# Performance work log

Hardware: AMD Instinct MI355X
Metric: run time of the kernel (lower is better)

The kernel has to match this reference:

```python
import jax, jax.numpy as jnp
import numpy as np

BN_EPS = 1e-6
SOFTMAX_EPS = 1e-8
D = 64      # fingerprint_dim
BD = 12     # bond_dim
N_ATOM = 10000
N_EDGE = 40000


def _bn(x, gamma, beta, mean, var):
    # BatchNorm1d in inference mode (running stats)
    return (x - mean) / jnp.sqrt(var + BN_EPS) * gamma + beta


def setup_inputs() -> dict:
    key = jax.random.key(0)
    ks = jax.random.split(key, 16)
    inp = {
        "atom": jax.random.normal(ks[0], (N_ATOM, D), dtype=jnp.float32),
        "bond_index": jax.random.randint(ks[1], (N_EDGE, 2), 0, N_ATOM, dtype=jnp.int64),
        "bond": jax.random.normal(ks[2], (N_EDGE, BD), dtype=jnp.float32),
        # encoder: Linear(bond_dim, D*D) + BatchNorm1d(D*D)
        "enc_W": jax.random.normal(ks[3], (D * D, BD), dtype=jnp.float32) * (1.0 / np.sqrt(BD)),
        "enc_b": jnp.zeros((D * D,), dtype=jnp.float32),
        "enc_gamma": jnp.ones((D * D,), dtype=jnp.float32),
        "enc_beta": jnp.zeros((D * D,), dtype=jnp.float32),
        "enc_mean": jnp.zeros((D * D,), dtype=jnp.float32),
        "enc_var": jnp.ones((D * D,), dtype=jnp.float32),
        # align: Linear(2*D, 1)
        "align_W": jax.random.normal(ks[4], (1, 2 * D), dtype=jnp.float32) * (1.0 / np.sqrt(2 * D)),
        "align_b": jnp.zeros((1,), dtype=jnp.float32),
        # attend: Linear(D, D) + BatchNorm1d(D), no activation
        "att_W": jax.random.normal(ks[5], (D, D), dtype=jnp.float32) * (1.0 / np.sqrt(D)),
        "att_b": jnp.zeros((D,), dtype=jnp.float32),
        "att_gamma": jnp.ones((D,), dtype=jnp.float32),
        "att_beta": jnp.zeros((D,), dtype=jnp.float32),
        "att_mean": jnp.zeros((D,), dtype=jnp.float32),
        "att_var": jnp.ones((D,), dtype=jnp.float32),
        # GRUCell(D, D)
        "gru_W_ih": jax.random.normal(ks[6], (3 * D, D), dtype=jnp.float32) * (1.0 / np.sqrt(D)),
        "gru_W_hh": jax.random.normal(ks[7], (3 * D, D), dtype=jnp.float32) * (1.0 / np.sqrt(D)),
        "gru_b_ih": jnp.zeros((3 * D,), dtype=jnp.float32),
        "gru_b_hh": jnp.zeros((3 * D,), dtype=jnp.float32),
    }
    return inp


def reference(atom, bond_index, bond,
              enc_W, enc_b, enc_gamma, enc_beta, enc_mean, enc_var,
              align_W, align_b,
              att_W, att_b, att_gamma, att_beta, att_mean, att_var,
              gru_W_ih, gru_W_hh, gru_b_ih, gru_b_hh):
    num_atom, d = atom.shape
    tgt = bond_index[:, 0]  # target atom of each edge
    nbr = bond_index[:, 1]  # neighbor atom of each edge

    # encoder: relu(BN(linear(bond))) -> per-edge [d, d] bond matrix
    enc = jax.nn.relu(_bn(bond @ enc_W.T + enc_b, enc_gamma, enc_beta, enc_mean, enc_var))
    enc = enc.reshape(-1, d, d)  # [E, d, d]

    # gather neighbor atoms, per-edge matvec through bond matrix
    neighbor = jnp.einsum('ed,edf->ef', atom[nbr], enc)  # [E, d]

    # attention logits (dropout is identity in eval)
    feat = jnp.concatenate([atom[tgt], neighbor], axis=-1)  # [E, 2d]
    score = jax.nn.leaky_relu(feat @ align_W.T + align_b, negative_slope=0.01)  # [E, 1]

    # segment softmax over target atoms
    mx = jax.ops.segment_max(score, tgt, num_segments=num_atom)  # [N, 1]
    ex = jnp.exp(score - mx[tgt])
    denom = jax.ops.segment_sum(ex, tgt, num_segments=num_atom)[tgt] + SOFTMAX_EPS
    attn = ex / denom  # [E, 1]

    # attend: BN(linear(neighbor)) (no activation), weighted scatter-add
    attd = _bn(neighbor @ att_W.T + att_b, att_gamma, att_beta, att_mean, att_var)
    context = jax.ops.segment_sum(attn * attd, tgt, num_segments=num_atom)  # [N, d]
    context = jax.nn.elu(context)

    # GRUCell(context, atom)
    gi = context @ gru_W_ih.T + gru_b_ih  # [N, 3d]
    gh = atom @ gru_W_hh.T + gru_b_hh     # [N, 3d]
    i_r, i_z, i_n = jnp.split(gi, 3, axis=-1)
    h_r, h_z, h_n = jnp.split(gh, 3, axis=-1)
    r = jax.nn.sigmoid(i_r + h_r)
    z = jax.nn.sigmoid(i_z + h_z)
    n = jnp.tanh(i_n + r * h_n)
    return (1.0 - z) * n + z * atom
```

## Files before the change

### kernel.cpp

```cpp
#include <hip/hip_runtime.h>
#include <math.h>

#define NA 10000
#define NE 40000

typedef float f4 __attribute__((ext_vector_type(4)));
typedef float f16v __attribute__((ext_vector_type(16)));
typedef int   i4 __attribute__((ext_vector_type(4)));
typedef __bf16 bf16x8 __attribute__((ext_vector_type(8)));

union U8 { unsigned short us[8]; bf16x8 v; };

static __device__ __forceinline__ unsigned short bf_rne(float x){
  unsigned u = __float_as_uint(x);
  unsigned r = (u + 0x7fffu + ((u>>16)&1u)) >> 16;
  return (unsigned short)r;
}
static __device__ __forceinline__ float bf_to_f(unsigned short h){
  return __uint_as_float(((unsigned)h)<<16);
}

__global__ __launch_bounds__(256) void k_pre(
  const float* __restrict__ encW, const float* __restrict__ encB,
  const float* __restrict__ eg, const float* __restrict__ ebt,
  const float* __restrict__ e_mn, const float* __restrict__ e_vr,
  const float* __restrict__ attW, const float* __restrict__ attB,
  const float* __restrict__ agm, const float* __restrict__ abt,
  const float* __restrict__ amn, const float* __restrict__ avr,
  const float* __restrict__ wih, const float* __restrict__ whh,
  const int* __restrict__ bidx, const float* __restrict__ atom,
  const float* __restrict__ alW,
  unsigned short* __restrict__ Bh, unsigned short* __restrict__ Bl,
  unsigned short* __restrict__ aBh, unsigned short* __restrict__ aBl,
  float* __restrict__ attBf, float* __restrict__ wT,
  float* __restrict__ p, int* __restrict__ cnt)
{
  int tid = threadIdx.x;
  int gid = blockIdx.x*256 + tid;
  int gstride = gridDim.x*256;
  for (int i=gid; i<65536; i+=gstride){
    int j = i&7, ll = (i>>3)&63, t = i>>9;
    int d = t>>1, ft = t&1;
    int k = ((ll>>5)<<3)+j;
    int n = d*64 + ft*32 + (ll&31);
    float s = eg[n]*rsqrtf(e_vr[n]+1e-6f);
    unsigned short vh=0, vl=0;
    if (k<12){
      float wv = encW[n*12+k]*s;
      unsigned short hi = bf_rne(wv);
      vh = hi; vl = bf_rne(wv - bf_to_f(hi));
    } else if (k==12){
      float b = (encB[n]-e_mn[n])*s + ebt[n];
      unsigned short hi = bf_rne(b);
      vh = hi; vl = bf_rne(b - bf_to_f(hi));
    }
    Bh[i] = vh; Bl[i] = vl;
  }
  for (int i=gid; i<4096; i+=gstride){
    int j=i&7, l=(i>>3)&63, t=i>>9;
    int kk=t>>1, nt=t&1;
    int k = kk*16 + ((l>>5)<<3) + j;
    int n = nt*32 + (l&31);
    float s = agm[n]*rsqrtf(avr[n]+1e-6f);
    float wv = attW[n*64+k]*s;
    unsigned short hi = bf_rne(wv);
    aBh[i]=hi; aBl[i]=bf_rne(wv - bf_to_f(hi));
  }
  for (int f=gid; f<64; f+=gstride){
    float s = agm[f]*rsqrtf(avr[f]+1e-6f);
    attBf[f] = (attB[f]-amn[f])*s + abt[f];
  }
  for (int i=gid; i<24576; i+=gstride){
    int j=i&3, f=(i>>2)&63, idx2=i>>8;
    int g=idx2>>4, kg=idx2&15, k=kg*4+j;
    wT[i] = (g<3)? wih[(g*64+f)*64+k] : whh[((g-3)*64+f)*64+k];
  }
  {
    int wid = gid>>6;
    int l = tid&63;
    float wl = alW[l];
    for (int a=wid; a<NA; a+=(gstride>>6)){
      float v = wl*atom[(size_t)a*64+l];
      v += __shfl_xor(v,1);  v += __shfl_xor(v,2);
      v += __shfl_xor(v,4);  v += __shfl_xor(v,8);
      v += __shfl_xor(v,16); v += __shfl_xor(v,32);
      if (l==0) p[a]=v;
    }
  }
  for (int e=gid; e<NE; e+=gstride) atomicAdd(&cnt[bidx[e*2]],1);
}

__global__ __launch_bounds__(256) void k_scan(const int* __restrict__ cnt,
                                              int* __restrict__ rowstart,
                                              int* __restrict__ wofs)
{
  __shared__ int sPart[256];
  int t = threadIdx.x;
  int base = t*40;
  i4 buf[10];
  int sum = 0;
  if (base < NA){
    const i4* cp = (const i4*)(cnt + base);
    #pragma unroll
    for (int i=0;i<10;i++) buf[i] = cp[i];
    #pragma unroll
    for (int i=0;i<10;i++) sum += buf[i].x+buf[i].y+buf[i].z+buf[i].w;
  }
  sPart[t]=sum;
  __syncthreads();
  for (int off=1; off<256; off<<=1){
    int v = (t>=off)? sPart[t-off] : 0;
    __syncthreads();
    sPart[t]+=v;
    __syncthreads();
  }
  int run = sPart[t]-sum;
  if (base < NA){
    #pragma unroll
    for (int i=0;i<10;i++){
      i4 b=buf[i], o;
      o.x=run; run+=b.x; o.y=run; run+=b.y;
      o.z=run; run+=b.z; o.w=run; run+=b.w;
      ((i4*)(rowstart+base))[i]=o;
      ((i4*)(wofs+base))[i]=o;
    }
  }
  if (t==0) rowstart[NA]=NE;
}

__global__ __launch_bounds__(256) void k_scatter(const int* __restrict__ bidx,
                                                 int* __restrict__ wofs,
                                                 int* __restrict__ elist)
{
  int e = blockIdx.x*256 + threadIdx.x;
  if (e < NE){
    int tg = bidx[e*2];
    int pos = atomicAdd(&wofs[tg],1);
    elist[pos]=e;
  }
}

__global__ __launch_bounds__(256) void k_edge(
  const float* __restrict__ atom, const int* __restrict__ bidx, const float* __restrict__ bond,
  const unsigned short* __restrict__ Bh, const unsigned short* __restrict__ Bl,
  const int* __restrict__ elist, float* __restrict__ nbC)
{
  __shared__ float sA[4352];
  __shared__ float sP[8192];
  __shared__ int   sEl[64];
  __shared__ int   sNbr[64];

  int tid = threadIdx.x;
  int l = tid & 63;
  int w = tid >> 6;
  int g = l >> 5;
  int em = l & 31;
  int E0 = blockIdx.x * 64;

  if (tid < 64){
    int e = elist[E0+tid];
    sEl[tid] = e;
    sNbr[tid] = bidx[e*2+1];
  }
  __syncthreads();
  for (int i=tid; i<4096; i+=256){
    int le=i>>6, d=i&63;
    sA[d*68+le] = atom[(size_t)sNbr[le]*64 + d];
  }

  U8 A1[2], A2[2];
  #pragma unroll
  for (int mt=0; mt<2; mt++){
    const f4* bp = (const f4*)(bond + (size_t)sEl[mt*32+em]*12);
    f4 b0=bp[0], b1v=bp[1], b2v=bp[2];
    float bv[12] = {b0.x,b0.y,b0.z,b0.w,b1v.x,b1v.y,b1v.z,b1v.w,b2v.x,b2v.y,b2v.z,b2v.w};
    unsigned short hi[12], lo2[12];
    #pragma unroll
    for (int j=0;j<12;j++){ hi[j]=bf_rne(bv[j]); lo2[j]=bf_rne(bv[j]-bf_to_f(hi[j])); }
    #pragma unroll
    for (int j=0;j<8;j++){
      int k = g*8+j;
      A1[mt].us[j] = (k<12)? hi[k] : (k==12? (unsigned short)0x3F80 : (unsigned short)0);
      A2[mt].us[j] = (k<12)? lo2[k] : (unsigned short)0;
    }
  }
  __syncthreads();

  f4 nacc[2][2][4];
  #pragma unroll
  for (int mt=0; mt<2; mt++)
    #pragma unroll
    for (int ft=0; ft<2; ft++)
      #pragma unroll
      for (int q=0;q<4;q++) nacc[mt][ft][q] = (f4){0.f,0.f,0.f,0.f};
  f16v cz;
  #pragma unroll
  for (int r=0;r<16;r++) cz[r] = 0.f;

  int dbase = w*16;
  U8 cbh0, cbl0, cbh1, cbl1;
  cbh0.v = *(const bf16x8*)(Bh + ((size_t)((dbase*2+0)*64 + l))*8);
  cbl0.v = *(const bf16x8*)(Bl + ((size_t)((dbase*2+0)*64 + l))*8);
  cbh1.v = *(const bf16x8*)(Bh + ((size_t)((dbase*2+1)*64 + l))*8);
  cbl1.v = *(const bf16x8*)(Bl + ((size_t)((dbase*2+1)*64 + l))*8);

  #pragma unroll 2
  for (int dd=0; dd<16; dd++){
    int d = dbase + dd;
    int dn = (dd<15)? d+1 : d;
    U8 nbh0, nbl0, nbh1, nbl1;
    nbh0.v = *(const bf16x8*)(Bh + ((size_t)((dn*2+0)*64 + l))*8);
    nbl0.v = *(const bf16x8*)(Bl + ((size_t)((dn*2+0)*64 + l))*8);
    nbh1.v = *(const bf16x8*)(Bh + ((size_t)((dn*2+1)*64 + l))*8);
    nbl1.v = *(const bf16x8*)(Bl + ((size_t)((dn*2+1)*64 + l))*8);

    #pragma unroll
    for (int mt=0; mt<2; mt++){
      f4 ldA[4];
      #pragma unroll
      for (int q=0;q<4;q++) ldA[q] = *(const f4*)&sA[d*68 + mt*32 + 8*q + 4*g];
      {
        f16v c;
        c = __builtin_amdgcn_mfma_f32_32x32x16_bf16(A1[mt].v, cbh0.v, cz, 0,0,0);
        c = __builtin_amdgcn_mfma_f32_32x32x16_bf16(A2[mt].v, cbh0.v, c, 0,0,0);
        c = __builtin_amdgcn_mfma_f32_32x32x16_bf16(A1[mt].v, cbl0.v, c, 0,0,0);
        #pragma unroll
        for (int r=0;r<16;r++){
          float ev = fmaxf(c[r], 0.f);
          nacc[mt][0][r>>2][r&3] = fmaf(ldA[r>>2][r&3], ev, nacc[mt][0][r>>2][r&3]);
        }
      }
      {
        f16v c;
        c = __builtin_amdgcn_mfma_f32_32x32x16_bf16(A1[mt].v, cbh1.v, cz, 0,0,0);
        c = __builtin_amdgcn_mfma_f32_32x32x16_bf16(A2[mt].v, cbh1.v, c, 0,0,0);
        c = __builtin_amdgcn_mfma_f32_32x32x16_bf16(A1[mt].v, cbl1.v, c, 0,0,0);
        #pragma unroll
        for (int r=0;r<16;r++){
          float ev = fmaxf(c[r], 0.f);
          nacc[mt][1][r>>2][r&3] = fmaf(ldA[r>>2][r&3], ev, nacc[mt][1][r>>2][r&3]);
        }
      }
    }
    cbh0 = nbh0; cbl0 = nbl0; cbh1 = nbh1; cbl1 = nbl1;
  }

  #pragma unroll
  for (int ft=0; ft<2; ft++){
    __syncthreads();
    #pragma unroll
    for (int mt=0; mt<2; mt++)
      #pragma unroll
      for (int r=0;r<16;r++)
        sP[w*2048 + mt*1024 + r*64 + l] = nacc[mt][ft][r>>2][r&3];
    __syncthreads();
    for (int idx=tid; idx<2048; idx+=256){
      float v = sP[idx] + sP[2048+idx] + sP[4096+idx] + sP[6144+idx];
      int mt = idx>>10, rl = idx&1023;
      int r = rl>>6, ll = rl&63;
      int m = mt*32 + (r&3) + ((r>>2)<<3) + ((ll>>5)<<2);
      int f = (ft<<5) + (ll&31);
      nbC[(size_t)(E0+m)*64 + f] = v;
    }
  }
}

__global__ __launch_bounds__(256) void k_zq(
  const float* __restrict__ nbC,
  const unsigned short* __restrict__ aBh, const unsigned short* __restrict__ aBl,
  const float* __restrict__ alW,
  float* __restrict__ zC, float* __restrict__ qv)
{
  __shared__ float sNb[64*68];
  int tid = threadIdx.x;
  int l = tid & 63;
  int w = tid >> 6;
  int g = l >> 5;
  int em = l & 31;
  int E0 = blockIdx.x * 64;

  for (int i=tid; i<4096; i+=256){
    int le=i>>6, f=i&63;
    sNb[le*68+f] = nbC[(size_t)(E0+le)*64 + f];
  }
  __syncthreads();

  {
    float alwn = alW[64+l];
    #pragma unroll 4
    for (int i=0;i<16;i++){
      int le = w*16 + i;
      float qq = sNb[le*68 + l] * alwn;
      qq += __shfl_xor(qq,1);  qq += __shfl_xor(qq,2);
      qq += __shfl_xor(qq,4);  qq += __shfl_xor(qq,8);
      qq += __shfl_xor(qq,16); qq += __shfl_xor(qq,32);
      if (l==0) qv[E0+le] = qq;
    }
  }

  {
    f16v c;
    #pragma unroll
    for (int r=0;r<16;r++) c[r] = 0.f;
    int mt2 = w>>1, nt = w&1;
    #pragma unroll
    for (int kk=0; kk<4; kk++){
      const float* src = &sNb[(mt2*32+em)*68 + kk*16 + g*8];
      f4 x0 = *(const f4*)src;
      f4 x1 = *(const f4*)(src+4);
      U8 Ah, Al;
      #pragma unroll
      for (int j=0;j<4;j++){
        unsigned short h0 = bf_rne(x0[j]);
        Ah.us[j] = h0; Al.us[j] = bf_rne(x0[j]-bf_to_f(h0));
        unsigned short h1 = bf_rne(x1[j]);
        Ah.us[4+j] = h1; Al.us[4+j] = bf_rne(x1[j]-bf_to_f(h1));
      }
      U8 bh, bl;
      bh.v = *(const bf16x8*)(aBh + ((size_t)((kk*2+nt)*64 + l))*8);
      bl.v = *(const bf16x8*)(aBl + ((size_t)((kk*2+nt)*64 + l))*8);
      c = __builtin_amdgcn_mfma_f32_32x32x16_bf16(Ah.v, bh.v, c, 0,0,0);
      c = __builtin_amdgcn_mfma_f32_32x32x16_bf16(Al.v, bh.v, c, 0,0,0);
      c = __builtin_amdgcn_mfma_f32_32x32x16_bf16(Ah.v, bl.v, c, 0,0,0);
    }
    #pragma unroll
    for (int r=0;r<16;r++){
      int row = (r&3) + ((r>>2)<<3) + ((l>>5)<<2);
      zC[(size_t)(E0 + mt2*32 + row)*64 + nt*32 + (l&31)] = c[r];
    }
  }
}

__global__ __launch_bounds__(256, 4) void k_gru(
  const float* __restrict__ atom, const float* __restrict__ zC,
  const int* __restrict__ rowstart, const float* __restrict__ p,
  const float* __restrict__ qv, const float* __restrict__ alB,
  const float* __restrict__ attBf, const float* __restrict__ wT,
  const float* __restrict__ bih, const float* __restrict__ bhh,
  float* __restrict__ out)
{
  __shared__ float sc[4][2][64];
  __shared__ float shh[4][2][64];
  int tid = threadIdx.x;
  int l = tid & 63;
  int w = tid >> 6;
  int base = blockIdx.x*8 + w*2;
  float bias = attBf[l];
  float ab = alB[0];

  #pragma unroll
  for (int aa=0; aa<2; aa++){
    int a = base + aa;
    float cf=0.f, hf=0.f;
    if (a < NA){
      hf = atom[(size_t)a*64 + l];
      int d0 = rowstart[a];
      int deg = rowstart[a+1] - d0;
      if (deg > 0){
        float pa = p[a] + ab;
        float mx = -1e30f;
        #pragma unroll 1
        for (int i=0;i<deg;i++){
          float s = pa + qv[d0+i];
          s = (s>0.f)? s : 0.01f*s;
          mx = fmaxf(mx, s);
        }
        float dn = 0.f, y = 0.f;
        #pragma unroll 1
        for (int i=0;i<deg;i++){
          float s = pa + qv[d0+i];
          s = (s>0.f)? s : 0.01f*s;
          float ex = __expf(s - mx);
          dn += ex;
          y = fmaf(ex, zC[(size_t)(d0+i)*64 + l], y);
        }
        cf = (y + dn*bias)/(dn + 1e-8f);
        cf = (cf>0.f)? cf : expm1f(cf);
      }
    }
    sc[w][aa][l] = cf; shh[w][aa][l] = hf;
  }
  __syncthreads();

  float acc[6][2];
  #pragma unroll
  for (int gg=0;gg<6;gg++){ acc[gg][0]=0.f; acc[gg][1]=0.f; }

  #pragma unroll 2
  for (int kg=0; kg<16; kg++){
    f4 wv[6];
    #pragma unroll
    for (int gg=0;gg<6;gg++) wv[gg] = *(const f4*)&wT[(size_t)((gg*16+kg)*64 + l)*4];
    #pragma unroll
    for (int aa=0;aa<2;aa++){
      f4 cv = *(const f4*)&sc[w][aa][kg*4];
      f4 hv = *(const f4*)&shh[w][aa][kg*4];
      #pragma unroll
      for (int j=0;j<4;j++){
        acc[0][aa] = fmaf(cv[j], wv[0][j], acc[0][aa]);
        acc[1][aa] = fmaf(cv[j], wv[1][j], acc[1][aa]);
        acc[2][aa] = fmaf(cv[j], wv[2][j], acc[2][aa]);
        acc[3][aa] = fmaf(hv[j], wv[3][j], acc[3][aa]);
        acc[4][aa] = fmaf(hv[j], wv[4][j], acc[4][aa]);
        acc[5][aa] = fmaf(hv[j], wv[5][j], acc[5][aa]);
      }
    }
  }

  float b0 = bih[l], b1 = bih[64+l], b2 = bih[128+l];
  float h0 = bhh[l], h1 = bhh[64+l], h2 = bhh[128+l];
  #pragma unroll
  for (int aa=0;aa<2;aa++){
    int a = base + aa;
    if (a < NA){
      float hf = shh[w][aa][l];
      float r = 1.f/(1.f + expf(-(acc[0][aa] + b0 + acc[3][aa] + h0)));
      float z = 1.f/(1.f + expf(-(acc[1][aa] + b1 + acc[4][aa] + h1)));
      float n = tanhf(acc[2][aa] + b2 + r*(acc[5][aa] + h2));
      out[(size_t)a*64 + l] = (1.f - z)*n + z*hf;
    }
  }
}

extern "C" void kernel_launch(void* const* d_in, const int* in_sizes, int n_in,
                              void* d_out, int out_size, void* d_ws, size_t ws_size,
                              hipStream_t stream) {
  const float* atom = (const float*)d_in[0];
  const int*   bidx = (const int*)  d_in[1];
  const float* bond = (const float*)d_in[2];
  const float* encW = (const float*)d_in[3];
  const float* encB = (const float*)d_in[4];
  const float* eg   = (const float*)d_in[5];
  const float* ebt  = (const float*)d_in[6];
  const float* e_mn = (const float*)d_in[7];
  const float* e_vr = (const float*)d_in[8];
  const float* alW  = (const float*)d_in[9];
  const float* alB  = (const float*)d_in[10];
  const float* atW  = (const float*)d_in[11];
  const float* atB  = (const float*)d_in[12];
  const float* agm  = (const float*)d_in[13];
  const float* abt  = (const float*)d_in[14];
  const float* amn  = (const float*)d_in[15];
  const float* avr  = (const float*)d_in[16];
  const float* wih  = (const float*)d_in[17];
  const float* whh  = (const float*)d_in[18];
  const float* bih  = (const float*)d_in[19];
  const float* bhh  = (const float*)d_in[20];

  float* ws = (float*)d_ws;
  unsigned short* Bh  = (unsigned short*)(ws + 0);
  unsigned short* Bl  = (unsigned short*)(ws + 32768);
  unsigned short* aBh = (unsigned short*)(ws + 65536);
  unsigned short* aBl = (unsigned short*)(ws + 67584);
  float* attBf   = ws + 69632;
  float* wT      = ws + 69696;
  float* p       = ws + 94272;
  int*   cnt     = (int*)(ws + 104288);
  int*   rowstart= (int*)(ws + 114304);
  int*   wofs    = (int*)(ws + 124320);
  int*   elist   = (int*)(ws + 134336);
  float* qv      = ws + 174336;
  float* nbC     = ws + 214336;
  float* outp    = (float*)d_out;

  hipMemsetAsync(cnt, 0, NA*sizeof(int), stream);
  k_pre<<<512, 256, 0, stream>>>(encW,encB,eg,ebt,e_mn,e_vr,
                                 atW,atB,agm,abt,amn,avr,
                                 wih,whh,bidx,atom,alW,
                                 Bh,Bl,aBh,aBl,attBf,wT,p,cnt);
  k_scan<<<1, 256, 0, stream>>>(cnt, rowstart, wofs);
  k_scatter<<<(NE+255)/256, 256, 0, stream>>>(bidx, wofs, elist);
  k_edge<<<625, 256, 0, stream>>>(atom, bidx, bond, Bh, Bl, elist, nbC);
  k_zq<<<625, 256, 0, stream>>>(nbC, aBh, aBl, alW, nbC , qv);
  k_gru<<<1250, 256, 0, stream>>>(atom, nbC, rowstart, p, qv, alB,
                                  attBf, wT, bih, bhh, outp);
}
```

Baseline: 188.0 us.

## Halve edges per block in k_edge and split waves across feature halves

```diff
diff --git a/kernel.cpp b/kernel.cpp
--- a/kernel.cpp
+++ b/kernel.cpp
@@ -145,33 +145,32 @@
   const unsigned short* __restrict__ Bh, const unsigned short* __restrict__ Bl,
   const int* __restrict__ elist, float* __restrict__ nbC)
 {
-  __shared__ float sA[4352];
-  __shared__ float sP[8192];
-  __shared__ int   sEl[64];
-  __shared__ int   sNbr[64];
+  __shared__ float sA[2304];
+  __shared__ float sP[4096];
+  __shared__ int   sEl[32];
+  __shared__ int   sNbr[32];
 
   int tid = threadIdx.x;
   int l = tid & 63;
   int w = tid >> 6;
   int g = l >> 5;
   int em = l & 31;
-  int E0 = blockIdx.x * 64;
-
-  if (tid < 64){
+  int E0 = blockIdx.x * 32;
+
+  if (tid < 32){
     int e = elist[E0+tid];
     sEl[tid] = e;
     sNbr[tid] = bidx[e*2+1];
   }
   __syncthreads();
-  for (int i=tid; i<4096; i+=256){
+  for (int i=tid; i<2048; i+=256){
     int le=i>>6, d=i&63;
-    sA[d*68+le] = atom[(size_t)sNbr[le]*64 + d];
-  }
-
-  U8 A1[2], A2[2];
-  #pragma unroll
-  for (int mt=0; mt<2; mt++){
-    const f4* bp = (const f4*)(bond + (size_t)sEl[mt*32+em]*12);
+    sA[d*36+le] = atom[(size_t)sNbr[le]*64 + d];
+  }
+
+  U8 A1, A2;
+  {
+    const f4* bp = (const f4*)(bond + (size_t)sEl[em]*12);
     f4 b0=bp[0], b1v=bp[1], b2v=bp[2];
     float bv[12] = {b0.x,b0.y,b0.z,b0.w,b1v.x,b1v.y,b1v.z,b1v.w,b2v.x,b2v.y,b2v.z,b2v.w};
     unsigned short hi[12], lo2[12];
@@ -180,86 +179,62 @@
     #pragma unroll
     for (int j=0;j<8;j++){
       int k = g*8+j;
-      A1[mt].us[j] = (k<12)? hi[k] : (k==12? (unsigned short)0x3F80 : (unsigned short)0);
-      A2[mt].us[j] = (k<12)? lo2[k] : (unsigned short)0;
-    }
-  }
-  __syncthreads();
-
-  f4 nacc[2][2][4];
-  #pragma unroll
-  for (int mt=0; mt<2; mt++)
-    #pragma unroll
-    for (int ft=0; ft<2; ft++)
-      #pragma unroll
-      for (int q=0;q<4;q++) nacc[mt][ft][q] = (f4){0.f,0.f,0.f,0.f};
+      A1.us[j] = (k<12)? hi[k] : (k==12? (unsigned short)0x3F80 : (unsigned short)0);
+      A2.us[j] = (k<12)? lo2[k] : (unsigned short)0;
+    }
+  }
+  __syncthreads();
+
+  int ft = w & 1;
+  int dbase = (w >> 1) * 32;
+
+  f4 nacc[4];
+  #pragma unroll
+  for (int q=0;q<4;q++) nacc[q] = (f4){0.f,0.f,0.f,0.f};
   f16v cz;
   #pragma unroll
   for (int r=0;r<16;r++) cz[r] = 0.f;
 
-  int dbase = w*16;
-  U8 cbh0, cbl0, cbh1, cbl1;
-  cbh0.v = *(const bf16x8*)(Bh + ((size_t)((dbase*2+0)*64 + l))*8);
-  cbl0.v = *(const bf16x8*)(Bl + ((size_t)((dbase*2+0)*64 + l))*8);
-  cbh1.v = *(const bf16x8*)(Bh + ((size_t)((dbase*2+1)*64 + l))*8);
-  cbl1.v = *(const bf16x8*)(Bl + ((size_t)((dbase*2+1)*64 + l))*8);
+  U8 cbh, cbl;
+  cbh.v = *(const bf16x8*)(Bh + ((size_t)((dbase*2+ft)*64 + l))*8);
+  cbl.v = *(const bf16x8*)(Bl + ((size_t)((dbase*2+ft)*64 + l))*8);
 
   #pragma unroll 2
-  for (int dd=0; dd<16; dd++){
+  for (int dd=0; dd<32; dd++){
     int d = dbase + dd;
-    int dn = (dd<15)? d+1 : d;
-    U8 nbh0, nbl0, nbh1, nbl1;
-    nbh0.v = *(const bf16x8*)(Bh + ((size_t)((dn*2+0)*64 + l))*8);
-    nbl0.v = *(const bf16x8*)(Bl + ((size_t)((dn*2+0)*64 + l))*8);
-    nbh1.v = *(const bf16x8*)(Bh + ((size_t)((dn*2+1)*64 + l))*8);
-    nbl1.v = *(const bf16x8*)(Bl + ((size_t)((dn*2+1)*64 + l))*8);
-
-    #pragma unroll
-    for (int mt=0; mt<2; mt++){
-      f4 ldA[4];
-      #pragma unroll
-      for (int q=0;q<4;q++) ldA[q] = *(const f4*)&sA[d*68 + mt*32 + 8*q + 4*g];
-      {
-        f16v c;
-        c = __builtin_amdgcn_mfma_f32_32x32x16_bf16(A1[mt].v, cbh0.v, cz, 0,0,0);
-        c = __builtin_amdgcn_mfma_f32_32x32x16_bf16(A2[mt].v, cbh0.v, c, 0,0,0);
-        c = __builtin_amdgcn_mfma_f32_32x32x16_bf16(A1[mt].v, cbl0.v, c, 0,0,0);
-        #pragma unroll
-        for (int r=0;r<16;r++){
-          float ev = fmaxf(c[r], 0.f);
-          nacc[mt][0][r>>2][r&3] = fmaf(ldA[r>>2][r&3], ev, nacc[mt][0][r>>2][r&3]);
-        }
-      }
-      {
-        f16v c;
-        c = __builtin_amdgcn_mfma_f32_32x32x16_bf16(A1[mt].v, cbh1.v, cz, 0,0,0);
-        c = __builtin_amdgcn_mfma_f32_32x32x16_bf16(A2[mt].v, cbh1.v, c, 0,0,0);
-        c = __builtin_amdgcn_mfma_f32_32x32x16_bf16(A1[mt].v, cbl1.v, c, 0,0,0);
-        #pragma unroll
-        for (int r=0;r<16;r++){
-          float ev = fmaxf(c[r], 0.f);
-          nacc[mt][1][r>>2][r&3] = fmaf(ldA[r>>2][r&3], ev, nacc[mt][1][r>>2][r&3]);
-        }
-      }
-    }
-    cbh0 = nbh0; cbl0 = nbl0; cbh1 = nbh1; cbl1 = nbl1;
-  }
-
-  #pragma unroll
-  for (int ft=0; ft<2; ft++){
-    __syncthreads();
-    #pragma unroll
-    for (int mt=0; mt<2; mt++)
-      #pragma unroll
-      for (int r=0;r<16;r++)
-        sP[w*2048 + mt*1024 + r*64 + l] = nacc[mt][ft][r>>2][r&3];
-    __syncthreads();
-    for (int idx=tid; idx<2048; idx+=256){
-      float v = sP[idx] + sP[2048+idx] + sP[4096+idx] + sP[6144+idx];
-      int mt = idx>>10, rl = idx&1023;
-      int r = rl>>6, ll = rl&63;
-      int m = mt*32 + (r&3) + ((r>>2)<<3) + ((ll>>5)<<2);
-      int f = (ft<<5) + (ll&31);
+    int dn = (dd<31)? d+1 : d;
+    U8 nbh, nbl;
+    nbh.v = *(const bf16x8*)(Bh + ((size_t)((dn*2+ft)*64 + l))*8);
+    nbl.v = *(const bf16x8*)(Bl + ((size_t)((dn*2+ft)*64 + l))*8);
+
+    f4 ldA[4];
+    #pragma unroll
+    for (int q=0;q<4;q++) ldA[q] = *(const f4*)&sA[d*36 + 8*q + 4*g];
+
+    f16v c;
+    c = __builtin_amdgcn_mfma_f32_32x32x16_bf16(A1.v, cbh.v, cz, 0,0,0);
+    c = __builtin_amdgcn_mfma_f32_32x32x16_bf16(A2.v, cbh.v, c, 0,0,0);
+    c = __builtin_amdgcn_mfma_f32_32x32x16_bf16(A1.v, cbl.v, c, 0,0,0);
+    #pragma unroll
+    for (int r=0;r<16;r++){
+      float ev = fmaxf(c[r], 0.f);
+      nacc[r>>2][r&3] = fmaf(ldA[r>>2][r&3], ev, nacc[r>>2][r&3]);
+    }
+    cbh = nbh; cbl = nbl;
+  }
+
+  #pragma unroll
+  for (int r=0;r<16;r++)
+    sP[w*1024 + r*64 + l] = nacc[r>>2][r&3];
+  __syncthreads();
+
+  if (w < 2){
+    #pragma unroll 4
+    for (int r=0;r<16;r++){
+      int idx = r*64 + l;
+      float v = sP[w*1024 + idx] + sP[(w+2)*1024 + idx];
+      int m = (r&3) + ((r>>2)<<3) + ((l>>5)<<2);
+      int f = (w<<5) + (l&31);
       nbC[(size_t)(E0+m)*64 + f] = v;
     }
   }
@@ -470,7 +445,7 @@
                                  Bh,Bl,aBh,aBl,attBf,wT,p,cnt);
   k_scan<<<1, 256, 0, stream>>>(cnt, rowstart, wofs);
   k_scatter<<<(NE+255)/256, 256, 0, stream>>>(bidx, wofs, elist);
-  k_edge<<<625, 256, 0, stream>>>(atom, bidx, bond, Bh, Bl, elist, nbC);
+  k_edge<<<1250, 256, 0, stream>>>(atom, bidx, bond, Bh, Bl, elist, nbC);
   k_zq<<<625, 256, 0, stream>>>(nbC, aBh, aBl, alW, nbC , qv);
   k_gru<<<1250, 256, 0, stream>>>(atom, nbC, rowstart, p, qv, alB,
                                   attBf, wT, bih, bhh, outp);
```

Result: no change. 186.6 us (-0.8%).
